# Kernel tuning notes

Measured on AMD Instinct MI355X. Metric: run time of the kernel, lower is better.

## Reference

```python
import jax, jax.numpy as jnp
import numpy as np

B, T, S = 4, 4096, 4096
D_MODEL = 512        # d_query = d_value_in = d_key_in
N_HEADS = 8
D_KEY = 512
D_VALUE = 512
N_OMEGA = 64
EPS = 1e-9
DK_H = D_KEY // N_HEADS      # 64
DV_H = D_VALUE // N_HEADS    # 64


def _glorot(key, shape):
    fan_in, fan_out = shape[-2], shape[-1]
    lim = np.sqrt(6.0 / (fan_in + fan_out))
    return jax.random.uniform(key, shape, jnp.float32, -lim, lim)


def _draw_omega(key, d_feature, n_omega):
    # n_omega == d_feature here -> single orthogonal block scaled by sqrt(d)
    g = jax.random.normal(key, (d_feature, d_feature), jnp.float32)
    q, _ = jnp.linalg.qr(g)
    q = q * jnp.sqrt(jnp.float32(d_feature))
    return q[:n_omega]


def setup_inputs() -> dict:
    key = jax.random.key(0)
    ks = jax.random.split(key, 7)
    return {
        "query": 0.5 * jax.random.normal(ks[0], (B, T, D_MODEL), jnp.float32),
        "value": 0.5 * jax.random.normal(ks[1], (B, S, D_MODEL), jnp.float32),
        "key": 0.5 * jax.random.normal(ks[2], (B, S, D_MODEL), jnp.float32),
        "wq": _glorot(ks[3], (N_HEADS, D_MODEL, DK_H)),
        "wv": _glorot(ks[4], (N_HEADS, D_MODEL, DV_H)),
        "wk": _glorot(ks[5], (N_HEADS, D_MODEL, DK_H)),
        "omega": _draw_omega(ks[6], DK_H, N_OMEGA),
    }


def _phi(x, omega):
    # x: (B,H,T,dk_h) -> (B,H,T,2*n_omega) FAVOR+ positive random features
    square_sum = 0.5 * jnp.sum(x * x, axis=-1, keepdims=True)
    xw = jnp.einsum('bhtk,mk->bhtm', x, omega)
    un = jnp.exp(jnp.concatenate([xw, -xw], axis=-1) - square_sum) + EPS
    return un / jnp.sqrt(jnp.float32(2.0 * N_OMEGA))


def reference(query, value, key, wq, wv, wk, omega):
    q = jnp.einsum('btf,hfk->bhtk', query, wq)   # (B,H,T,dk_h)
    v = jnp.einsum('bsd,hdk->bhsk', value, wv)   # (B,H,S,dv_h)
    k = jnp.einsum('bsf,hfk->bhsk', key, wk)     # (B,H,S,dk_h)
    qp = _phi(q, omega)                          # (B,H,T,2M)
    kp = _phi(k, omega)                          # (B,H,S,2M)
    v1 = jnp.concatenate([v, jnp.ones(v.shape[:-1] + (1,), v.dtype)], axis=-1)
    kv = jnp.einsum('bhsm,bhsd->bhmd', kp, v1)   # (B,H,2M,dv_h+1)
    qkv = jnp.einsum('bhtm,bhmd->bhtd', qp, kv)  # (B,H,T,dv_h+1)
    normalizer = qkv[..., -1:]
    out = qkv[..., :-1] / normalizer
    # faithful to original: plain reshape (B,H,T,dv_h) -> (B,T,D_VALUE), no transpose
    return jnp.reshape(out, (B, T, D_VALUE))
```

## Files before the change

### kernel.cpp

```cpp
#include <hip/hip_runtime.h>

typedef _Float16 half8 __attribute__((ext_vector_type(8)));
typedef _Float16 half4_t __attribute__((ext_vector_type(4)));
typedef short short8 __attribute__((ext_vector_type(8)));
typedef unsigned short u16x4 __attribute__((ext_vector_type(4)));
typedef float f32x4 __attribute__((ext_vector_type(4)));

#define NH 8

__device__ __forceinline__ unsigned short f2bf(float x) {
  union { float f; unsigned u; } v; v.f = x;
  unsigned r = v.u + 0x7FFFu + ((v.u >> 16) & 1u);
  return (unsigned short)(r >> 16);
}

__global__ __launch_bounds__(256) void k0_qk(
    const float* __restrict__ wq, const float* __restrict__ wk,
    const float* __restrict__ omega,
    _Float16* __restrict__ wxq, _Float16* __restrict__ wxk) {
  const int bid = blockIdx.x;
  const int arr = bid >> 7;
  const int h = (bid >> 4) & 7;
  const int ft = (bid >> 1) & 7;
  const int os = bid & 1;
  const int f = threadIdx.x & 63;
  const int w = threadIdx.x >> 6;
  const float* wsrc = (arr ? wk : wq) + ((size_t)h * 512 + ft * 64 + f) * 64;
  float wreg[64];
#pragma unroll
  for (int i = 0; i < 16; ++i) {
    float4 v = *(const float4*)(wsrc + i * 4);
    wreg[i * 4] = v.x; wreg[i * 4 + 1] = v.y; wreg[i * 4 + 2] = v.z; wreg[i * 4 + 3] = v.w;
  }
  _Float16* outp = arr ? wxk : wxq;
  const int k8 = f >> 3, e = f & 7;
#pragma unroll 1
  for (int oo = 0; oo < 8; ++oo) {
    const int o = w * 16 + os * 8 + oo;
    const float* om = omega + o * 64;
    float s = 0.f;
#pragma unroll
    for (int k = 0; k < 64; ++k) s = fmaf(wreg[k], om[k], s);
    outp[((((size_t)h * 8 + ft) * 8 + k8) * 64 + o) * 8 + e] = (_Float16)s;
  }
}

__global__ __launch_bounds__(256) void k0_v(
    const float* __restrict__ wv, _Float16* __restrict__ wvt) {
  int idx = blockIdx.x * 256 + threadIdx.x;
  int h = idx >> 15, o = (idx >> 9) & 63, f = idx & 511;
  float val = wv[((size_t)h * 512 + f) * 64 + o];
  wvt[((((size_t)h * 8 + (f >> 6)) * 8 + ((f >> 3) & 7)) * 64 + o) * 8 + (f & 7)] = (_Float16)val;
}

__global__ __launch_bounds__(512, 4) void fused_kv(
    const float* __restrict__ key, const float* __restrict__ value,
    const _Float16* __restrict__ wxk, const _Float16* __restrict__ wvt,
    float* __restrict__ kvpart) {
  __shared__ __align__(16) _Float16 A[128][72];
  __shared__ __align__(16) _Float16 W[4096];
  __shared__ __align__(16) unsigned short kpT[128][136];
  __shared__ __align__(16) unsigned short vT[64][136];
  const int bid = blockIdx.x;
  const int h = bid >> 6;
  const int b = (bid >> 4) & 3;
  const int sc = bid & 15;
  const int s0 = sc * 256;
  const int bh = b * NH + h;
  const int tid = threadIdx.x;
  const int w = tid >> 6;
  const int lane = tid & 63;
  const int g = lane >> 4, c = lane & 15;
  const int xr = lane >> 4;
  const int xc = (lane & 15) * 4;

  short8 bones;
#pragma unroll
  for (int i = 0; i < 8; ++i) bones[i] = (c == 0) ? (short)0x3F80 : (short)0;

  f32x4 acc_kv[5];
#pragma unroll
  for (int j = 0; j < 5; ++j) acc_kv[j] = (f32x4){0.f, 0.f, 0.f, 0.f};

  const float* xb0 = key + (size_t)(b * 4096 + s0 + w * 16 + xr) * 512 + xc;
  const _Float16* wb0 = wxk + (size_t)h * 32768;
  float4 xv[4];
  half8 wr;
#pragma unroll
  for (int i = 0; i < 4; ++i) xv[i] = *(const float4*)(xb0 + i * 2048);
  wr = *(const half8*)(wb0 + tid * 8);

#pragma unroll 1
  for (int p = 0; p < 4; ++p) {
    const float* xb = ((p & 1) ? value : key) +
                      (size_t)(b * 4096 + s0 + (p >> 1) * 128 + w * 16 + xr) * 512 + xc;
    const _Float16* wb = ((p & 1) ? wvt : wxk) + (size_t)h * 32768;

    f32x4 accp[4];
#pragma unroll
    for (int j = 0; j < 4; ++j) accp[j] = (f32x4){0.f, 0.f, 0.f, 0.f};

#pragma unroll 1
    for (int kc = 0; kc < 8; ++kc) {
      asm volatile("s_waitcnt lgkmcnt(0)" ::: "memory");
      __builtin_amdgcn_s_barrier();
      __builtin_amdgcn_sched_barrier(0);
#pragma unroll
      for (int i = 0; i < 4; ++i) {
        float vv[4] = {xv[i].x, xv[i].y, xv[i].z, xv[i].w};
        half4_t hv;
#pragma unroll
        for (int j2 = 0; j2 < 4; ++j2) hv[j2] = (_Float16)vv[j2];
        *(half4_t*)&A[w * 16 + i * 4 + xr][xc] = hv;
      }
      *(half8*)&W[tid * 8] = wr;
      if (kc < 7) {
#pragma unroll
        for (int i = 0; i < 4; ++i)
          xv[i] = *(const float4*)(xb + (kc + 1) * 64 + i * 2048);
        wr = *(const half8*)(wb + (kc + 1) * 4096 + tid * 8);
      } else if (p < 3) {
        const int pn = p + 1;
        const float* xb2 = ((pn & 1) ? value : key) +
                           (size_t)(b * 4096 + s0 + (pn >> 1) * 128 + w * 16 + xr) * 512 + xc;
        const _Float16* wb2 = ((pn & 1) ? wvt : wxk) + (size_t)h * 32768;
#pragma unroll
        for (int i = 0; i < 4; ++i) xv[i] = *(const float4*)(xb2 + i * 2048);
        wr = *(const half8*)(wb2 + tid * 8);
      }
      asm volatile("s_waitcnt lgkmcnt(0)" ::: "memory");
      __builtin_amdgcn_s_barrier();
      __builtin_amdgcn_sched_barrier(0);
#pragma unroll
      for (int ks = 0; ks < 2; ++ks) {
        half8 a = *(const half8*)&A[w * 16 + c][ks * 32 + g * 8];
#pragma unroll
        for (int nf = 0; nf < 4; ++nf) {
          half8 bf = *(const half8*)&W[((ks * 4 + g) * 64 + nf * 16 + c) * 8];
          accp[nf] = __builtin_amdgcn_mfma_f32_16x16x32_f16(a, bf, accp[nf], 0, 0, 0);
        }
      }
    }

    const int sl0 = w * 16 + g * 4;
    if ((p & 1) == 0) {
      float ss_[4];
#pragma unroll
      for (int j = 0; j < 4; ++j) {
        float s = 0.f;
#pragma unroll
        for (int nf = 0; nf < 4; ++nf) { float q = accp[nf][j]; s = fmaf(q, q, s); }
        s += __shfl_xor(s, 1); s += __shfl_xor(s, 2);
        s += __shfl_xor(s, 4); s += __shfl_xor(s, 8);
        ss_[j] = s * 0.0078125f;
      }
#pragma unroll
      for (int nf = 0; nf < 4; ++nf) {
        const int m = nf * 16 + c;
        u16x4 kp_p, kp_m;
#pragma unroll
        for (int j = 0; j < 4; ++j) {
          float v = accp[nf][j];
          kp_p[j] = f2bf(__expf(v - ss_[j]) + 1e-9f);
          kp_m[j] = f2bf(__expf(-v - ss_[j]) + 1e-9f);
        }
        *(u16x4*)&kpT[m][sl0] = kp_p;
        *(u16x4*)&kpT[64 + m][sl0] = kp_m;
      }
    } else {
#pragma unroll
      for (int nf = 0; nf < 4; ++nf) {
        u16x4 vv;
#pragma unroll
        for (int j = 0; j < 4; ++j) vv[j] = f2bf(accp[nf][j]);
        *(u16x4*)&vT[nf * 16 + c][sl0] = vv;
      }
      asm volatile("s_waitcnt lgkmcnt(0)" ::: "memory");
      __builtin_amdgcn_s_barrier();
      __builtin_amdgcn_sched_barrier(0);
#pragma unroll
      for (int ks = 0; ks < 4; ++ks) {
        short8 a = *(const short8*)&kpT[w * 16 + c][ks * 32 + g * 8];
#pragma unroll
        for (int nf = 0; nf < 4; ++nf) {
          short8 bb = *(const short8*)&vT[nf * 16 + c][ks * 32 + g * 8];
          acc_kv[nf] = __builtin_amdgcn_mfma_f32_16x16x32_bf16(a, bb, acc_kv[nf], 0, 0, 0);
        }
        acc_kv[4] = __builtin_amdgcn_mfma_f32_16x16x32_bf16(a, bones, acc_kv[4], 0, 0, 0);
      }
      __builtin_amdgcn_s_barrier();
    }
  }

  float* pbase = kvpart + ((size_t)sc * 32 + bh) * 10240;
#pragma unroll
  for (int nf = 0; nf < 5; ++nf)
#pragma unroll
    for (int j = 0; j < 4; ++j) {
      int m = w * 16 + g * 4 + j;
      pbase[m * 80 + nf * 16 + c] = acc_kv[nf][j];
    }
}

__global__ __launch_bounds__(128) void k3a_denom(
    const float* __restrict__ kvpart, float* __restrict__ invbuf,
    float* __restrict__ lsc) {
  const int bh = blockIdx.x;
  const int m = threadIdx.x;
  const float* base = kvpart + (size_t)bh * 10240 + m * 80 + 64;
  float s = 0.f;
#pragma unroll
  for (int kk = 0; kk < 16; ++kk) s += base[(size_t)kk * 327680];
  invbuf[bh * 128 + m] = 1.0f / s;
  lsc[bh * 128 + m] = __logf(s);
}

__global__ __launch_bounds__(256) void k3b_reduce(
    const float* __restrict__ kvpart, const float* __restrict__ invbuf,
    _Float16* __restrict__ kvnt) {
  const int bh = blockIdx.x;
  const int e0 = blockIdx.y * 1024 + threadIdx.x * 4;
  const int m = e0 / 80;
  const int d0 = e0 - m * 80;
  const float* base = kvpart + (size_t)bh * 10240 + e0;
  f32x4 s = (f32x4){0.f, 0.f, 0.f, 0.f};
#pragma unroll
  for (int kk = 0; kk < 16; ++kk) {
    f32x4 v = *(const f32x4*)(base + (size_t)kk * 327680);
    s += v;
  }
  const float inv = invbuf[bh * 128 + m];
  const int mst = ((m & 63) << 1) | (m >> 6);
  _Float16* outb = kvnt + (size_t)bh * 10240 + mst;
#pragma unroll
  for (int j = 0; j < 4; ++j) {
    const int d = d0 + j;
    float val;
    if (d < 64) val = s[j] * inv;
    else if (d == 64) val = 1.0f;
    else val = 0.f;
    outb[d * 128] = (_Float16)val;
  }
}

__global__ __launch_bounds__(512, 4) void fused_qo(
    const float* __restrict__ query, const _Float16* __restrict__ wxq,
    const _Float16* __restrict__ kvnt, const float* __restrict__ lsc,
    float* __restrict__ out) {
  __shared__ __align__(16) _Float16 A[128][72];
  __shared__ __align__(16) _Float16 W[4096];
  __shared__ __align__(16) _Float16 qpT[128][136];
  const int bid = blockIdx.x;
  const int h = bid >> 7;
  const int rt = bid & 127;
  const int R0 = rt * 128;
  const int b = R0 >> 12;
  const int t0 = R0 & 4095;
  const int bh = b * NH + h;
  const int tid = threadIdx.x;
  const int w = tid >> 6;
  const int lane = tid & 63;
  const int g = lane >> 4, c = lane & 15;
  const int xr = lane >> 4;
  const int xc = (lane & 15) * 4;

  const float* xb = query + (size_t)(b * 4096 + t0 + w * 16 + xr) * 512 + xc;
  const _Float16* wb = wxq + (size_t)h * 32768;

  float4 xv[4];
  half8 wr;
#pragma unroll
  for (int i = 0; i < 4; ++i) xv[i] = *(const float4*)(xb + i * 2048);
  wr = *(const half8*)(wb + tid * 8);

  f32x4 accp[4];
#pragma unroll
  for (int j = 0; j < 4; ++j) accp[j] = (f32x4){0.f, 0.f, 0.f, 0.f};

#pragma unroll 1
  for (int kc = 0; kc < 8; ++kc) {
    asm volatile("s_waitcnt lgkmcnt(0)" ::: "memory");
    __builtin_amdgcn_s_barrier();
    __builtin_amdgcn_sched_barrier(0);
#pragma unroll
    for (int i = 0; i < 4; ++i) {
      float vv[4] = {xv[i].x, xv[i].y, xv[i].z, xv[i].w};
      half4_t hv;
#pragma unroll
      for (int j2 = 0; j2 < 4; ++j2) hv[j2] = (_Float16)vv[j2];
      *(half4_t*)&A[w * 16 + i * 4 + xr][xc] = hv;
    }
    *(half8*)&W[tid * 8] = wr;
    if (kc < 7) {
#pragma unroll
      for (int i = 0; i < 4; ++i)
        xv[i] = *(const float4*)(xb + (kc + 1) * 64 + i * 2048);
      wr = *(const half8*)(wb + (size_t)(kc + 1) * 4096 + tid * 8);
    }
    asm volatile("s_waitcnt lgkmcnt(0)" ::: "memory");
    __builtin_amdgcn_s_barrier();
    __builtin_amdgcn_sched_barrier(0);
#pragma unroll
    for (int ks = 0; ks < 2; ++ks) {
      half8 a = *(const half8*)&A[w * 16 + c][ks * 32 + g * 8];
#pragma unroll
      for (int nf = 0; nf < 4; ++nf) {
        half8 bf = *(const half8*)&W[((ks * 4 + g) * 64 + nf * 16 + c) * 8];
        accp[nf] = __builtin_amdgcn_mfma_f32_16x16x32_f16(a, bf, accp[nf], 0, 0, 0);
      }
    }
  }

  float Lp[4], Lm[4];
#pragma unroll
  for (int nf = 0; nf < 4; ++nf) {
    Lp[nf] = lsc[bh * 128 + nf * 16 + c];
    Lm[nf] = lsc[bh * 128 + 64 + nf * 16 + c];
  }
  float ss_[4], cm_[4];
#pragma unroll
  for (int j = 0; j < 4; ++j) {
    float s = 0.f;
#pragma unroll
    for (int nf = 0; nf < 4; ++nf) { float q = accp[nf][j]; s = fmaf(q, q, s); }
    s += __shfl_xor(s, 1); s += __shfl_xor(s, 2);
    s += __shfl_xor(s, 4); s += __shfl_xor(s, 8);
    ss_[j] = s * 0.0078125f;
  }
#pragma unroll
  for (int j = 0; j < 4; ++j) {
    float m0 = -1e30f;
#pragma unroll
    for (int nf = 0; nf < 4; ++nf) {
      float v = accp[nf][j];
      m0 = fmaxf(m0, fmaxf(v - ss_[j] + Lp[nf], -v - ss_[j] + Lm[nf]));
      m0 = fmaxf(m0, fmaxf(Lp[nf], Lm[nf]) - 20.723265f);
    }
    m0 = fmaxf(m0, __shfl_xor(m0, 1)); m0 = fmaxf(m0, __shfl_xor(m0, 2));
    m0 = fmaxf(m0, __shfl_xor(m0, 4)); m0 = fmaxf(m0, __shfl_xor(m0, 8));
    cm_[j] = m0;
  }
#pragma unroll
  for (int nf = 0; nf < 4; ++nf) {
    const int m = nf * 16 + c;
#pragma unroll
    for (int j = 0; j < 4; ++j) {
      float v = accp[nf][j];
      _Float16 pp = (_Float16)(__expf(v - ss_[j] + Lp[nf] - cm_[j]) +
                               1e-9f * __expf(Lp[nf] - cm_[j]));
      _Float16 pm = (_Float16)(__expf(-v - ss_[j] + Lm[nf] - cm_[j]) +
                               1e-9f * __expf(Lm[nf] - cm_[j]));
      union { unsigned u; _Float16 hh[2]; } pk;
      pk.hh[0] = pp; pk.hh[1] = pm;
      *(unsigned*)&qpT[w * 16 + g * 4 + j][2 * m] = pk.u;
    }
  }
  asm volatile("s_waitcnt lgkmcnt(0)" ::: "memory");
  __builtin_amdgcn_s_barrier();
  __builtin_amdgcn_sched_barrier(0);

  f32x4 acco[5];
#pragma unroll
  for (int j = 0; j < 5; ++j) acco[j] = (f32x4){0.f, 0.f, 0.f, 0.f};
  const _Float16* kvb = kvnt + (size_t)bh * 10240;
#pragma unroll
  for (int ks = 0; ks < 4; ++ks) {
    half8 a = *(const half8*)&qpT[w * 16 + c][ks * 32 + g * 8];
#pragma unroll
    for (int nf = 0; nf < 5; ++nf) {
      half8 bb = *(const half8*)(kvb + (size_t)(nf * 16 + c) * 128 + ks * 32 + g * 8);
      acco[nf] = __builtin_amdgcn_mfma_f32_16x16x32_f16(a, bb, acco[nf], 0, 0, 0);
    }
  }
  const int tb = t0 + w * 16 + g * 4;
#pragma unroll
  for (int j = 0; j < 4; ++j) {
    float nrm = __shfl(acco[4][j], (lane & 48));
    float invn = 1.0f / nrm;
#pragma unroll
    for (int nf = 0; nf < 4; ++nf) {
      out[((size_t)bh * 4096 + tb + j) * 64 + nf * 16 + c] = acco[nf][j] * invn;
    }
  }
}

extern "C" void kernel_launch(void* const* d_in, const int* in_sizes, int n_in,
                              void* d_out, int out_size, void* d_ws, size_t ws_size,
                              hipStream_t stream) {
  const float* query = (const float*)d_in[0];
  const float* value = (const float*)d_in[1];
  const float* key   = (const float*)d_in[2];
  const float* wq    = (const float*)d_in[3];
  const float* wv    = (const float*)d_in[4];
  const float* wk    = (const float*)d_in[5];
  const float* omega = (const float*)d_in[6];
  float* out = (float*)d_out;
  char* ws = (char*)d_ws;

  _Float16* wxq  = (_Float16*)(ws);
  _Float16* wxk  = (_Float16*)(ws + 524288);
  _Float16* wvt  = (_Float16*)(ws + 1048576);
  float* kvpart  = (float*)(ws + 1572864);
  _Float16* kvnt = (_Float16*)(ws + 22544384);
  float* lsc     = (float*)(ws + 23199744);
  float* invbuf  = (float*)(ws + 23216128);

  k0_qk<<<256, 256, 0, stream>>>(wq, wk, omega, wxq, wxk);
  k0_v<<<1024, 256, 0, stream>>>(wv, wvt);
  fused_kv<<<512, 512, 0, stream>>>(key, value, wxk, wvt, kvpart);
  k3a_denom<<<32, 128, 0, stream>>>(kvpart, invbuf, lsc);
  k3b_reduce<<<dim3(32, 10), 256, 0, stream>>>(kvpart, invbuf, kvnt);
  fused_qo<<<1024, 512, 0, stream>>>(query, wxq, kvnt, lsc, out);
}
```

Baseline: 113.4 us.

## Process two heads per block with double-buffered LDS staging in projection kernels

Both fused_kv and fused_qo now handle a pair of heads per workgroup, so each input row tile (key/value/query) is loaded from global memory and converted to fp16 once and reused for two heads' weight slices. This halves the redundant activation reads. The per-chunk staging is also double-buffered in LDS, so each k-chunk needs one barrier instead of two and the next tile's stores overlap with the current MFMAs. In exchange, LDS use roughly doubles, launch bounds drop to one block per CU, grid sizes halve, and the head-pair epilogue serialises through shared kpT/vT/qpT buffers with extra barriers.

```diff
diff --git a/kernel.cpp b/kernel.cpp
--- a/kernel.cpp
+++ b/kernel.cpp
@@ -13,6 +13,11 @@
   unsigned r = v.u + 0x7FFFu + ((v.u >> 16) & 1u);
   return (unsigned short)(r >> 16);
 }
+
+#define DRAIN_BAR()                                  \
+  asm volatile("s_waitcnt lgkmcnt(0)" ::: "memory"); \
+  __builtin_amdgcn_s_barrier();                      \
+  __builtin_amdgcn_sched_barrier(0)
 
 __global__ __launch_bounds__(256) void k0_qk(
     const float* __restrict__ wq, const float* __restrict__ wk,
@@ -53,153 +58,193 @@
   wvt[((((size_t)h * 8 + (f >> 6)) * 8 + ((f >> 3) & 7)) * 64 + o) * 8 + (f & 7)] = (_Float16)val;
 }
 
-__global__ __launch_bounds__(512, 4) void fused_kv(
+__global__ __launch_bounds__(512, 1) void fused_kv(
     const float* __restrict__ key, const float* __restrict__ value,
     const _Float16* __restrict__ wxk, const _Float16* __restrict__ wvt,
     float* __restrict__ kvpart) {
-  __shared__ __align__(16) _Float16 A[128][72];
-  __shared__ __align__(16) _Float16 W[4096];
+  __shared__ __align__(16) _Float16 A[2][128][72];
+  __shared__ __align__(16) _Float16 W[2][2][4096];
   __shared__ __align__(16) unsigned short kpT[128][136];
   __shared__ __align__(16) unsigned short vT[64][136];
   const int bid = blockIdx.x;
-  const int h = bid >> 6;
+  const int hp = bid >> 6;
   const int b = (bid >> 4) & 3;
   const int sc = bid & 15;
   const int s0 = sc * 256;
-  const int bh = b * NH + h;
   const int tid = threadIdx.x;
   const int w = tid >> 6;
   const int lane = tid & 63;
   const int g = lane >> 4, c = lane & 15;
+  const int hh = w >> 2;
+  const int rq = w & 3;
   const int xr = lane >> 4;
   const int xc = (lane & 15) * 4;
 
+  const _Float16* wkb0 = wxk + (size_t)(hp * 2) * 32768;
+  const _Float16* wkb1 = wkb0 + 32768;
+  const _Float16* wvb0 = wvt + (size_t)(hp * 2) * 32768;
+  const _Float16* wvb1 = wvb0 + 32768;
+
   short8 bones;
 #pragma unroll
   for (int i = 0; i < 8; ++i) bones[i] = (c == 0) ? (short)0x3F80 : (short)0;
 
-  f32x4 acc_kv[5];
-#pragma unroll
-  for (int j = 0; j < 5; ++j) acc_kv[j] = (f32x4){0.f, 0.f, 0.f, 0.f};
-
-  const float* xb0 = key + (size_t)(b * 4096 + s0 + w * 16 + xr) * 512 + xc;
-  const _Float16* wb0 = wxk + (size_t)h * 32768;
+  f32x4 acc_kv[2][5];
+#pragma unroll
+  for (int h2 = 0; h2 < 2; ++h2)
+#pragma unroll
+    for (int j = 0; j < 5; ++j) acc_kv[h2][j] = (f32x4){0.f, 0.f, 0.f, 0.f};
+
+  u16x4 kps[2][4], kms[2][4], vs_[2][4];
+
   float4 xv[4];
-  half8 wr;
-#pragma unroll
-  for (int i = 0; i < 4; ++i) xv[i] = *(const float4*)(xb0 + i * 2048);
-  wr = *(const half8*)(wb0 + tid * 8);
+  half8 wr0, wr1;
 
 #pragma unroll 1
   for (int p = 0; p < 4; ++p) {
     const float* xb = ((p & 1) ? value : key) +
                       (size_t)(b * 4096 + s0 + (p >> 1) * 128 + w * 16 + xr) * 512 + xc;
-    const _Float16* wb = ((p & 1) ? wvt : wxk) + (size_t)h * 32768;
-
-    f32x4 accp[4];
-#pragma unroll
-    for (int j = 0; j < 4; ++j) accp[j] = (f32x4){0.f, 0.f, 0.f, 0.f};
+    const _Float16* wb0 = (p & 1) ? wvb0 : wkb0;
+    const _Float16* wb1 = (p & 1) ? wvb1 : wkb1;
+
+#pragma unroll
+    for (int i = 0; i < 4; ++i) xv[i] = *(const float4*)(xb + i * 2048);
+    wr0 = *(const half8*)(wb0 + tid * 8);
+    wr1 = *(const half8*)(wb1 + tid * 8);
+#pragma unroll
+    for (int i = 0; i < 4; ++i) {
+      float vv[4] = {xv[i].x, xv[i].y, xv[i].z, xv[i].w};
+      half4_t hv;
+#pragma unroll
+      for (int j2 = 0; j2 < 4; ++j2) hv[j2] = (_Float16)vv[j2];
+      *(half4_t*)&A[0][w * 16 + i * 4 + xr][xc] = hv;
+    }
+    *(half8*)&W[0][0][tid * 8] = wr0;
+    *(half8*)&W[0][1][tid * 8] = wr1;
+#pragma unroll
+    for (int i = 0; i < 4; ++i) xv[i] = *(const float4*)(xb + 64 + i * 2048);
+    wr0 = *(const half8*)(wb0 + 4096 + tid * 8);
+    wr1 = *(const half8*)(wb1 + 4096 + tid * 8);
+    DRAIN_BAR();
+
+    f32x4 accp[2][4];
+#pragma unroll
+    for (int mf = 0; mf < 2; ++mf)
+#pragma unroll
+      for (int j = 0; j < 4; ++j) accp[mf][j] = (f32x4){0.f, 0.f, 0.f, 0.f};
 
 #pragma unroll 1
     for (int kc = 0; kc < 8; ++kc) {
-      asm volatile("s_waitcnt lgkmcnt(0)" ::: "memory");
-      __builtin_amdgcn_s_barrier();
-      __builtin_amdgcn_sched_barrier(0);
-#pragma unroll
-      for (int i = 0; i < 4; ++i) {
-        float vv[4] = {xv[i].x, xv[i].y, xv[i].z, xv[i].w};
-        half4_t hv;
-#pragma unroll
-        for (int j2 = 0; j2 < 4; ++j2) hv[j2] = (_Float16)vv[j2];
-        *(half4_t*)&A[w * 16 + i * 4 + xr][xc] = hv;
-      }
-      *(half8*)&W[tid * 8] = wr;
+      const int cur = kc & 1;
       if (kc < 7) {
-#pragma unroll
-        for (int i = 0; i < 4; ++i)
-          xv[i] = *(const float4*)(xb + (kc + 1) * 64 + i * 2048);
-        wr = *(const half8*)(wb + (kc + 1) * 4096 + tid * 8);
-      } else if (p < 3) {
-        const int pn = p + 1;
-        const float* xb2 = ((pn & 1) ? value : key) +
-                           (size_t)(b * 4096 + s0 + (pn >> 1) * 128 + w * 16 + xr) * 512 + xc;
-        const _Float16* wb2 = ((pn & 1) ? wvt : wxk) + (size_t)h * 32768;
-#pragma unroll
-        for (int i = 0; i < 4; ++i) xv[i] = *(const float4*)(xb2 + i * 2048);
-        wr = *(const half8*)(wb2 + tid * 8);
-      }
-      asm volatile("s_waitcnt lgkmcnt(0)" ::: "memory");
-      __builtin_amdgcn_s_barrier();
-      __builtin_amdgcn_sched_barrier(0);
+        const int nxt = cur ^ 1;
+#pragma unroll
+        for (int i = 0; i < 4; ++i) {
+          float vv[4] = {xv[i].x, xv[i].y, xv[i].z, xv[i].w};
+          half4_t hv;
+#pragma unroll
+          for (int j2 = 0; j2 < 4; ++j2) hv[j2] = (_Float16)vv[j2];
+          *(half4_t*)&A[nxt][w * 16 + i * 4 + xr][xc] = hv;
+        }
+        *(half8*)&W[nxt][0][tid * 8] = wr0;
+        *(half8*)&W[nxt][1][tid * 8] = wr1;
+        if (kc < 6) {
+#pragma unroll
+          for (int i = 0; i < 4; ++i)
+            xv[i] = *(const float4*)(xb + (kc + 2) * 64 + i * 2048);
+          wr0 = *(const half8*)(wb0 + (kc + 2) * 4096 + tid * 8);
+          wr1 = *(const half8*)(wb1 + (kc + 2) * 4096 + tid * 8);
+        }
+      }
 #pragma unroll
       for (int ks = 0; ks < 2; ++ks) {
-        half8 a = *(const half8*)&A[w * 16 + c][ks * 32 + g * 8];
+        half8 af0 = *(const half8*)&A[cur][rq * 32 + c][ks * 32 + g * 8];
+        half8 af1 = *(const half8*)&A[cur][rq * 32 + 16 + c][ks * 32 + g * 8];
 #pragma unroll
         for (int nf = 0; nf < 4; ++nf) {
-          half8 bf = *(const half8*)&W[((ks * 4 + g) * 64 + nf * 16 + c) * 8];
-          accp[nf] = __builtin_amdgcn_mfma_f32_16x16x32_f16(a, bf, accp[nf], 0, 0, 0);
-        }
-      }
-    }
-
-    const int sl0 = w * 16 + g * 4;
+          half8 wf = *(const half8*)&W[cur][hh][((ks * 4 + g) * 64 + nf * 16 + c) * 8];
+          accp[0][nf] = __builtin_amdgcn_mfma_f32_16x16x32_f16(af0, wf, accp[0][nf], 0, 0, 0);
+          accp[1][nf] = __builtin_amdgcn_mfma_f32_16x16x32_f16(af1, wf, accp[1][nf], 0, 0, 0);
+        }
+      }
+      DRAIN_BAR();
+    }
+
     if ((p & 1) == 0) {
-      float ss_[4];
-#pragma unroll
-      for (int j = 0; j < 4; ++j) {
-        float s = 0.f;
-#pragma unroll
-        for (int nf = 0; nf < 4; ++nf) { float q = accp[nf][j]; s = fmaf(q, q, s); }
-        s += __shfl_xor(s, 1); s += __shfl_xor(s, 2);
-        s += __shfl_xor(s, 4); s += __shfl_xor(s, 8);
-        ss_[j] = s * 0.0078125f;
-      }
-#pragma unroll
-      for (int nf = 0; nf < 4; ++nf) {
-        const int m = nf * 16 + c;
-        u16x4 kp_p, kp_m;
+#pragma unroll
+      for (int mf = 0; mf < 2; ++mf) {
+        float ss_[4];
 #pragma unroll
         for (int j = 0; j < 4; ++j) {
-          float v = accp[nf][j];
-          kp_p[j] = f2bf(__expf(v - ss_[j]) + 1e-9f);
-          kp_m[j] = f2bf(__expf(-v - ss_[j]) + 1e-9f);
-        }
-        *(u16x4*)&kpT[m][sl0] = kp_p;
-        *(u16x4*)&kpT[64 + m][sl0] = kp_m;
+          float s = 0.f;
+#pragma unroll
+          for (int nf = 0; nf < 4; ++nf) { float q = accp[mf][nf][j]; s = fmaf(q, q, s); }
+          s += __shfl_xor(s, 1); s += __shfl_xor(s, 2);
+          s += __shfl_xor(s, 4); s += __shfl_xor(s, 8);
+          ss_[j] = s * 0.0078125f;
+        }
+#pragma unroll
+        for (int nf = 0; nf < 4; ++nf) {
+          u16x4 kp_p, kp_m;
+#pragma unroll
+          for (int j = 0; j < 4; ++j) {
+            float v = accp[mf][nf][j];
+            kp_p[j] = f2bf(__expf(v - ss_[j]) + 1e-9f);
+            kp_m[j] = f2bf(__expf(-v - ss_[j]) + 1e-9f);
+          }
+          kps[mf][nf] = kp_p;
+          kms[mf][nf] = kp_m;
+        }
       }
     } else {
 #pragma unroll
-      for (int nf = 0; nf < 4; ++nf) {
-        u16x4 vv;
-#pragma unroll
-        for (int j = 0; j < 4; ++j) vv[j] = f2bf(accp[nf][j]);
-        *(u16x4*)&vT[nf * 16 + c][sl0] = vv;
-      }
-      asm volatile("s_waitcnt lgkmcnt(0)" ::: "memory");
-      __builtin_amdgcn_s_barrier();
-      __builtin_amdgcn_sched_barrier(0);
-#pragma unroll
-      for (int ks = 0; ks < 4; ++ks) {
-        short8 a = *(const short8*)&kpT[w * 16 + c][ks * 32 + g * 8];
+      for (int mf = 0; mf < 2; ++mf)
 #pragma unroll
         for (int nf = 0; nf < 4; ++nf) {
-          short8 bb = *(const short8*)&vT[nf * 16 + c][ks * 32 + g * 8];
-          acc_kv[nf] = __builtin_amdgcn_mfma_f32_16x16x32_bf16(a, bb, acc_kv[nf], 0, 0, 0);
-        }
-        acc_kv[4] = __builtin_amdgcn_mfma_f32_16x16x32_bf16(a, bones, acc_kv[4], 0, 0, 0);
-      }
-      __builtin_amdgcn_s_barrier();
-    }
-  }
-
-  float* pbase = kvpart + ((size_t)sc * 32 + bh) * 10240;
-#pragma unroll
-  for (int nf = 0; nf < 5; ++nf)
-#pragma unroll
-    for (int j = 0; j < 4; ++j) {
-      int m = w * 16 + g * 4 + j;
-      pbase[m * 80 + nf * 16 + c] = acc_kv[nf][j];
-    }
+          u16x4 vv;
+#pragma unroll
+          for (int j = 0; j < 4; ++j) vv[j] = f2bf(accp[mf][nf][j]);
+          vs_[mf][nf] = vv;
+        }
+#pragma unroll
+      for (int h2 = 0; h2 < 2; ++h2) {
+        if (hh == h2) {
+#pragma unroll
+          for (int mf = 0; mf < 2; ++mf)
+#pragma unroll
+            for (int nf = 0; nf < 4; ++nf) {
+              const int m = nf * 16 + c;
+              const int sl = rq * 32 + mf * 16 + g * 4;
+              *(u16x4*)&kpT[m][sl] = kps[mf][nf];
+              *(u16x4*)&kpT[64 + m][sl] = kms[mf][nf];
+              *(u16x4*)&vT[m][sl] = vs_[mf][nf];
+            }
+        }
+        DRAIN_BAR();
+#pragma unroll
+        for (int ks = 0; ks < 4; ++ks) {
+          short8 a = *(const short8*)&kpT[w * 16 + c][ks * 32 + g * 8];
+#pragma unroll
+          for (int nf = 0; nf < 4; ++nf) {
+            short8 bb = *(const short8*)&vT[nf * 16 + c][ks * 32 + g * 8];
+            acc_kv[h2][nf] = __builtin_amdgcn_mfma_f32_16x16x32_bf16(a, bb, acc_kv[h2][nf], 0, 0, 0);
+          }
+          acc_kv[h2][4] = __builtin_amdgcn_mfma_f32_16x16x32_bf16(a, bones, acc_kv[h2][4], 0, 0, 0);
+        }
+        __builtin_amdgcn_s_barrier();
+      }
+    }
+  }
+
+#pragma unroll
+  for (int h2 = 0; h2 < 2; ++h2) {
+    float* pbase = kvpart + ((size_t)sc * 32 + b * 8 + hp * 2 + h2) * 10240;
+#pragma unroll
+    for (int nf = 0; nf < 5; ++nf)
+#pragma unroll
+      for (int j = 0; j < 4; ++j)
+        pbase[(w * 16 + g * 4 + j) * 80 + nf * 16 + c] = acc_kv[h2][nf][j];
+  }
 }
 
 __global__ __launch_bounds__(128) void k3a_denom(
@@ -243,144 +288,173 @@
   }
 }
 
-__global__ __launch_bounds__(512, 4) void fused_qo(
+__global__ __launch_bounds__(512, 1) void fused_qo(
     const float* __restrict__ query, const _Float16* __restrict__ wxq,
     const _Float16* __restrict__ kvnt, const float* __restrict__ lsc,
     float* __restrict__ out) {
-  __shared__ __align__(16) _Float16 A[128][72];
-  __shared__ __align__(16) _Float16 W[4096];
+  __shared__ __align__(16) _Float16 A[2][128][72];
+  __shared__ __align__(16) _Float16 W[2][2][4096];
   __shared__ __align__(16) _Float16 qpT[128][136];
   const int bid = blockIdx.x;
-  const int h = bid >> 7;
+  const int hp = bid >> 7;
   const int rt = bid & 127;
-  const int R0 = rt * 128;
-  const int b = R0 >> 12;
-  const int t0 = R0 & 4095;
-  const int bh = b * NH + h;
+  const int b = rt >> 5;
+  const int t0 = (rt & 31) * 128;
   const int tid = threadIdx.x;
   const int w = tid >> 6;
   const int lane = tid & 63;
   const int g = lane >> 4, c = lane & 15;
+  const int hh = w >> 2;
+  const int rq = w & 3;
   const int xr = lane >> 4;
   const int xc = (lane & 15) * 4;
 
-  const float* xb = query + (size_t)(b * 4096 + t0 + w * 16 + xr) * 512 + xc;
-  const _Float16* wb = wxq + (size_t)h * 32768;
+  const float* xb = query + (size_t)(rt * 128 + w * 16 + xr) * 512 + xc;
+  const _Float16* wb0 = wxq + (size_t)(hp * 2) * 32768;
+  const _Float16* wb1 = wb0 + 32768;
 
   float4 xv[4];
-  half8 wr;
+  half8 wr0, wr1;
 #pragma unroll
   for (int i = 0; i < 4; ++i) xv[i] = *(const float4*)(xb + i * 2048);
-  wr = *(const half8*)(wb + tid * 8);
-
-  f32x4 accp[4];
-#pragma unroll
-  for (int j = 0; j < 4; ++j) accp[j] = (f32x4){0.f, 0.f, 0.f, 0.f};
+  wr0 = *(const half8*)(wb0 + tid * 8);
+  wr1 = *(const half8*)(wb1 + tid * 8);
+#pragma unroll
+  for (int i = 0; i < 4; ++i) {
+    float vv[4] = {xv[i].x, xv[i].y, xv[i].z, xv[i].w};
+    half4_t hv;
+#pragma unroll
+    for (int j2 = 0; j2 < 4; ++j2) hv[j2] = (_Float16)vv[j2];
+    *(half4_t*)&A[0][w * 16 + i * 4 + xr][xc] = hv;
+  }
+  *(half8*)&W[0][0][tid * 8] = wr0;
+  *(half8*)&W[0][1][tid * 8] = wr1;
+#pragma unroll
+  for (int i = 0; i < 4; ++i) xv[i] = *(const float4*)(xb + 64 + i * 2048);
+  wr0 = *(const half8*)(wb0 + 4096 + tid * 8);
+  wr1 = *(const half8*)(wb1 + 4096 + tid * 8);
+  DRAIN_BAR();
+
+  f32x4 accp[2][4];
+#pragma unroll
+  for (int mf = 0; mf < 2; ++mf)
+#pragma unroll
+    for (int j = 0; j < 4; ++j) accp[mf][j] = (f32x4){0.f, 0.f, 0.f, 0.f};
 
 #pragma unroll 1
   for (int kc = 0; kc < 8; ++kc) {
-    asm volatile("s_waitcnt lgkmcnt(0)" ::: "memory");
+    const int cur = kc & 1;
+    if (kc < 7) {
+      const int nxt = cur ^ 1;
+#pragma unroll
+      for (int i = 0; i < 4; ++i) {
+        float vv[4] = {xv[i].x, xv[i].y, xv[i].z, xv[i].w};
+        half4_t hv;
+#pragma unroll
+        for (int j2 = 0; j2 < 4; ++j2) hv[j2] = (_Float16)vv[j2];
+        *(half4_t*)&A[nxt][w * 16 + i * 4 + xr][xc] = hv;
+      }
+      *(half8*)&W[nxt][0][tid * 8] = wr0;
+      *(half8*)&W[nxt][1][tid * 8] = wr1;
+      if (kc < 6) {
+#pragma unroll
+        for (int i = 0; i < 4; ++i)
+          xv[i] = *(const float4*)(xb + (kc + 2) * 64 + i * 2048);
+        wr0 = *(const half8*)(wb0 + (kc + 2) * 4096 + tid * 8);
+        wr1 = *(const half8*)(wb1 + (kc + 2) * 4096 + tid * 8);
+      }
+    }
+#pragma unroll
+    for (int ks = 0; ks < 2; ++ks) {
+      half8 af0 = *(const half8*)&A[cur][rq * 32 + c][ks * 32 + g * 8];
+      half8 af1 = *(const half8*)&A[cur][rq * 32 + 16 + c][ks * 32 + g * 8];
+#pragma unroll
+      for (int nf = 0; nf < 4; ++nf) {
+        half8 wf = *(const half8*)&W[cur][hh][((ks * 4 + g) * 64 + nf * 16 + c) * 8];
+        accp[0][nf] = __builtin_amdgcn_mfma_f32_16x16x32_f16(af0, wf, accp[0][nf], 0, 0, 0);
+        accp[1][nf] = __builtin_amdgcn_mfma_f32_16x16x32_f16(af1, wf, accp[1][nf], 0, 0, 0);
+      }
+    }
+    DRAIN_BAR();
+  }
+
+#pragma unroll
+  for (int h2 = 0; h2 < 2; ++h2) {
+    const int bh = b * 8 + hp * 2 + h2;
+    if (hh == h2) {
+      float Lp[4], Lm[4];
+#pragma unroll
+      for (int nf = 0; nf < 4; ++nf) {
+        Lp[nf] = lsc[bh * 128 + nf * 16 + c];
+        Lm[nf] = lsc[bh * 128 + 64 + nf * 16 + c];
+      }
+#pragma unroll
+      for (int mf = 0; mf < 2; ++mf) {
+        float ss_[4], cm_[4];
+#pragma unroll
+        for (int j = 0; j < 4; ++j) {
+          float s = 0.f;
+#pragma unroll
+          for (int nf = 0; nf < 4; ++nf) { float q = accp[mf][nf][j]; s = fmaf(q, q, s); }
+          s += __shfl_xor(s, 1); s += __shfl_xor(s, 2);
+          s += __shfl_xor(s, 4); s += __shfl_xor(s, 8);
+          ss_[j] = s * 0.0078125f;
+        }
+#pragma unroll
+        for (int j = 0; j < 4; ++j) {
+          float m0 = -1e30f;
+#pragma unroll
+          for (int nf = 0; nf < 4; ++nf) {
+            float v = accp[mf][nf][j];
+            m0 = fmaxf(m0, fmaxf(v - ss_[j] + Lp[nf], -v - ss_[j] + Lm[nf]));
+            m0 = fmaxf(m0, fmaxf(Lp[nf], Lm[nf]) - 20.723265f);
+          }
+          m0 = fmaxf(m0, __shfl_xor(m0, 1)); m0 = fmaxf(m0, __shfl_xor(m0, 2));
+          m0 = fmaxf(m0, __shfl_xor(m0, 4)); m0 = fmaxf(m0, __shfl_xor(m0, 8));
+          cm_[j] = m0;
+        }
+#pragma unroll
+        for (int nf = 0; nf < 4; ++nf) {
+          const int m = nf * 16 + c;
+#pragma unroll
+          for (int j = 0; j < 4; ++j) {
+            float v = accp[mf][nf][j];
+            _Float16 pp = (_Float16)(__expf(v - ss_[j] + Lp[nf] - cm_[j]) +
+                                     1e-9f * __expf(Lp[nf] - cm_[j]));
+            _Float16 pm = (_Float16)(__expf(-v - ss_[j] + Lm[nf] - cm_[j]) +
+                                     1e-9f * __expf(Lm[nf] - cm_[j]));
+            union { unsigned u; _Float16 hhx[2]; } pk;
+            pk.hhx[0] = pp; pk.hhx[1] = pm;
+            *(unsigned*)&qpT[rq * 32 + mf * 16 + g * 4 + j][2 * m] = pk.u;
+          }
+        }
+      }
+    }
+    DRAIN_BAR();
+    f32x4 acco[5];
+#pragma unroll
+    for (int j = 0; j < 5; ++j) acco[j] = (f32x4){0.f, 0.f, 0.f, 0.f};
+    const _Float16* kvb = kvnt + (size_t)bh * 10240;
+#pragma unroll
+    for (int ks = 0; ks < 4; ++ks) {
+      half8 a = *(const half8*)&qpT[w * 16 + c][ks * 32 + g * 8];
+#pragma unroll
+      for (int nf = 0; nf < 5; ++nf) {
+        half8 bb = *(const half8*)(kvb + (size_t)(nf * 16 + c) * 128 + ks * 32 + g * 8);
+        acco[nf] = __builtin_amdgcn_mfma_f32_16x16x32_f16(a, bb, acco[nf], 0, 0, 0);
+      }
+    }
+    const int tb = t0 + w * 16 + g * 4;
+#pragma unroll
+    for (int j = 0; j < 4; ++j) {
+      float nrm = __shfl(acco[4][j], (lane & 48));
+      float invn = 1.0f / nrm;
+#pragma unroll
+      for (int nf = 0; nf < 4; ++nf) {
+        out[((size_t)bh * 4096 + tb + j) * 64 + nf * 16 + c] = acco[nf][j] * invn;
+      }
+    }
     __builtin_amdgcn_s_barrier();
-    __builtin_amdgcn_sched_barrier(0);
-#pragma unroll
-    for (int i = 0; i < 4; ++i) {
-      float vv[4] = {xv[i].x, xv[i].y, xv[i].z, xv[i].w};
-      half4_t hv;
-#pragma unroll
-      for (int j2 = 0; j2 < 4; ++j2) hv[j2] = (_Float16)vv[j2];
-      *(half4_t*)&A[w * 16 + i * 4 + xr][xc] = hv;
-    }
-    *(half8*)&W[tid * 8] = wr;
-    if (kc < 7) {
-#pragma unroll
-      for (int i = 0; i < 4; ++i)
-        xv[i] = *(const float4*)(xb + (kc + 1) * 64 + i * 2048);
-      wr = *(const half8*)(wb + (size_t)(kc + 1) * 4096 + tid * 8);
-    }
-    asm volatile("s_waitcnt lgkmcnt(0)" ::: "memory");
-    __builtin_amdgcn_s_barrier();
-    __builtin_amdgcn_sched_barrier(0);
-#pragma unroll
-    for (int ks = 0; ks < 2; ++ks) {
-      half8 a = *(const half8*)&A[w * 16 + c][ks * 32 + g * 8];
-#pragma unroll
-      for (int nf = 0; nf < 4; ++nf) {
-        half8 bf = *(const half8*)&W[((ks * 4 + g) * 64 + nf * 16 + c) * 8];
-        accp[nf] = __builtin_amdgcn_mfma_f32_16x16x32_f16(a, bf, accp[nf], 0, 0, 0);
-      }
-    }
-  }
-
-  float Lp[4], Lm[4];
-#pragma unroll
-  for (int nf = 0; nf < 4; ++nf) {
-    Lp[nf] = lsc[bh * 128 + nf * 16 + c];
-    Lm[nf] = lsc[bh * 128 + 64 + nf * 16 + c];
-  }
-  float ss_[4], cm_[4];
-#pragma unroll
-  for (int j = 0; j < 4; ++j) {
-    float s = 0.f;
-#pragma unroll
-    for (int nf = 0; nf < 4; ++nf) { float q = accp[nf][j]; s = fmaf(q, q, s); }
-    s += __shfl_xor(s, 1); s += __shfl_xor(s, 2);
-    s += __shfl_xor(s, 4); s += __shfl_xor(s, 8);
-    ss_[j] = s * 0.0078125f;
-  }
-#pragma unroll
-  for (int j = 0; j < 4; ++j) {
-    float m0 = -1e30f;
-#pragma unroll
-    for (int nf = 0; nf < 4; ++nf) {
-      float v = accp[nf][j];
-      m0 = fmaxf(m0, fmaxf(v - ss_[j] + Lp[nf], -v - ss_[j] + Lm[nf]));
-      m0 = fmaxf(m0, fmaxf(Lp[nf], Lm[nf]) - 20.723265f);
-    }
-    m0 = fmaxf(m0, __shfl_xor(m0, 1)); m0 = fmaxf(m0, __shfl_xor(m0, 2));
-    m0 = fmaxf(m0, __shfl_xor(m0, 4)); m0 = fmaxf(m0, __shfl_xor(m0, 8));
-    cm_[j] = m0;
-  }
-#pragma unroll
-  for (int nf = 0; nf < 4; ++nf) {
-    const int m = nf * 16 + c;
-#pragma unroll
-    for (int j = 0; j < 4; ++j) {
-      float v = accp[nf][j];
-      _Float16 pp = (_Float16)(__expf(v - ss_[j] + Lp[nf] - cm_[j]) +
-                               1e-9f * __expf(Lp[nf] - cm_[j]));
-      _Float16 pm = (_Float16)(__expf(-v - ss_[j] + Lm[nf] - cm_[j]) +
-                               1e-9f * __expf(Lm[nf] - cm_[j]));
-      union { unsigned u; _Float16 hh[2]; } pk;
-      pk.hh[0] = pp; pk.hh[1] = pm;
-      *(unsigned*)&qpT[w * 16 + g * 4 + j][2 * m] = pk.u;
-    }
-  }
-  asm volatile("s_waitcnt lgkmcnt(0)" ::: "memory");
-  __builtin_amdgcn_s_barrier();
-  __builtin_amdgcn_sched_barrier(0);
-
-  f32x4 acco[5];
-#pragma unroll
-  for (int j = 0; j < 5; ++j) acco[j] = (f32x4){0.f, 0.f, 0.f, 0.f};
-  const _Float16* kvb = kvnt + (size_t)bh * 10240;
-#pragma unroll
-  for (int ks = 0; ks < 4; ++ks) {
-    half8 a = *(const half8*)&qpT[w * 16 + c][ks * 32 + g * 8];
-#pragma unroll
-    for (int nf = 0; nf < 5; ++nf) {
-      half8 bb = *(const half8*)(kvb + (size_t)(nf * 16 + c) * 128 + ks * 32 + g * 8);
-      acco[nf] = __builtin_amdgcn_mfma_f32_16x16x32_f16(a, bb, acco[nf], 0, 0, 0);
-    }
-  }
-  const int tb = t0 + w * 16 + g * 4;
-#pragma unroll
-  for (int j = 0; j < 4; ++j) {
-    float nrm = __shfl(acco[4][j], (lane & 48));
-    float invn = 1.0f / nrm;
-#pragma unroll
-    for (int nf = 0; nf < 4; ++nf) {
-      out[((size_t)bh * 4096 + tb + j) * 64 + nf * 16 + c] = acco[nf][j] * invn;
-    }
   }
 }
 
@@ -407,8 +481,8 @@
 
   k0_qk<<<256, 256, 0, stream>>>(wq, wk, omega, wxq, wxk);
   k0_v<<<1024, 256, 0, stream>>>(wv, wvt);
-  fused_kv<<<512, 512, 0, stream>>>(key, value, wxk, wvt, kvpart);
+  fused_kv<<<256, 512, 0, stream>>>(key, value, wxk, wvt, kvpart);
   k3a_denom<<<32, 128, 0, stream>>>(kvpart, invbuf, lsc);
   k3b_reduce<<<dim3(32, 10), 256, 0, stream>>>(kvpart, invbuf, kvnt);
-  fused_qo<<<1024, 512, 0, stream>>>(query, wxq, kvnt, lsc, out);
-}
+  fused_qo<<<512, 512, 0, stream>>>(query, wxq, kvnt, lsc, out);
+}
```

Result: slower. 115.8 us (+2.1%).
